# Kernel optimization log

Measured on AMD Instinct MI355X. Metric: run time of the kernel, lower is better.

Reference implementation:

```python
import jax, jax.numpy as jnp
import numpy as np
from math import sqrt

D = 512        # output_dim (layer_dims[-1])
H = 4          # num_heads
ATN = D // H   # atn_dim = 128
BERT_D = 768
B = 32         # number of graph pairs
NP = 4096
NH = 4096


def setup_inputs() -> dict:
    key = jax.random.key(0)
    ks = jax.random.split(key, 20)
    inp = {
        'ctx_p': jax.random.normal(ks[0], (NP, D), jnp.float32),
        'ctx_h': jax.random.normal(ks[1], (NH, D), jnp.float32),
        'lhs_p': jax.random.normal(ks[2], (NP, BERT_D), jnp.float32),
        'lhs_h': jax.random.normal(ks[3], (NH, BERT_D), jnp.float32),
        'batch_p': jnp.sort(jax.random.randint(ks[4], (NP,), 0, B)).astype(jnp.int64),
        'batch_h': jnp.sort(jax.random.randint(ks[5], (NH,), 0, B)).astype(jnp.int64),
        # learned parameters (stored [in, out])
        'Wq': jax.random.normal(ks[6], (D, D), jnp.float32) * 0.02,
        'bq': jnp.zeros((D,), jnp.float32),
        'Wk': jax.random.normal(ks[7], (D, D), jnp.float32) * 0.02,
        'bk': jnp.zeros((D,), jnp.float32),
        'Wv': jax.random.normal(ks[8], (BERT_D, BERT_D), jnp.float32) * 0.02,
        'bv': jnp.zeros((BERT_D,), jnp.float32),
        'W1': jax.random.normal(ks[9], (D + BERT_D, 256), jnp.float32) * 0.02,
        'b1': jnp.zeros((256,), jnp.float32),
        'W2': jax.random.normal(ks[10], (256, 128), jnp.float32) * 0.02,
        'ln_g': jnp.ones((128,), jnp.float32),
        'ln_b': jnp.zeros((128,), jnp.float32),
        'Wc': jax.random.normal(ks[11], (128, 3), jnp.float32) * 0.02,
        'bc': jnp.zeros((3,), jnp.float32),
    }
    return inp


def reference(ctx_p, ctx_h, lhs_p, lhs_h, batch_p, batch_h,
              Wq, bq, Wk, bk, Wv, bv, W1, b1, W2, ln_g, ln_b, Wc, bc):
    # q/k projections; torch code does .view(-1, atn_dim, num_heads) -> head is fastest axis
    qs = (ctx_h @ Wq + bq).reshape(-1, ATN, H)          # [nh, atn, H]
    ks = (ctx_p @ Wk + bk).reshape(-1, ATN, H)          # [np, atn, H]
    vs = (lhs_p @ Wv + bv).reshape(-1, H, BERT_D // H)  # [np, H, 768/H]

    atn = jnp.einsum('ndh,mdh->nmh', qs, ks) / sqrt(ATN)  # [nh, np, H]
    # faithful to original: positions where batch ids MATCH are set to -1e10
    mask_same = batch_h[:, None] == batch_p[None, :]       # [nh, np]
    atn = jnp.where(mask_same[:, :, None], jnp.float32(-1e10), atn)
    atn = jax.nn.softmax(atn, axis=1)                      # softmax over premise words m

    attended = jnp.einsum('nmh,mhd->nhd', atn, vs).reshape(-1, BERT_D)  # [nh, 768]

    feats = jnp.concatenate([ctx_h, lhs_h - attended], axis=1)  # [nh, D+768]
    h1 = jax.nn.gelu(feats @ W1 + b1, approximate=False)
    h2 = h1 @ W2                                                # Linear no bias
    mu = h2.mean(axis=-1, keepdims=True)
    var = ((h2 - mu) ** 2).mean(axis=-1, keepdims=True)
    h2 = (h2 - mu) * jax.lax.rsqrt(var + 1e-5) * ln_g + ln_b    # LayerNorm(128)

    # global_mean_pool over batch_h
    pooled = jax.ops.segment_sum(h2, batch_h, num_segments=B)
    counts = jax.ops.segment_sum(jnp.ones((h2.shape[0], 1), h2.dtype), batch_h, num_segments=B)
    pooled = pooled / jnp.maximum(counts, 1.0)

    return pooled @ Wc + bc  # [B, 3]
```

## Files before the change

kernel.cpp:

```cpp
#include <hip/hip_runtime.h>
#include <hip/hip_bf16.h>
#include <math.h>

#define NP_N 4096
#define NH_N 4096
#define D_N 512
#define BERT_N 768
#define H_N 4
#define B_N 32
#define SCL2 0.12754245006257576f

typedef __attribute__((ext_vector_type(8))) short short8;
typedef __attribute__((ext_vector_type(4))) float f32x4;
typedef __attribute__((ext_vector_type(4))) unsigned short ush4;
typedef __attribute__((ext_vector_type(4))) unsigned int uivec4;
typedef unsigned short ushort_t;

__device__ __forceinline__ void gl_lds16(const void* g, void* l) {
    __builtin_amdgcn_global_load_lds((const __attribute__((address_space(1))) void*)g,
                                     (__attribute__((address_space(3))) void*)l, 16, 0, 0);
}
__device__ __forceinline__ unsigned short f2bu(float f) {
    __hip_bfloat16 b = __float2bfloat16(f);
    return *reinterpret_cast<unsigned short*>(&b);
}
__device__ __forceinline__ float b2f(unsigned short u) {
    union { unsigned int i; float f; } x; x.i = ((unsigned int)u) << 16; return x.f;
}
__device__ __forceinline__ unsigned int pkbf(float a, float b) {
    union { __hip_bfloat162 h; unsigned int u; } x;
    x.h.x = __float2bfloat16(a);
    x.h.y = __float2bfloat16(b);
    return x.u;
}
__device__ __forceinline__ unsigned int sxor(unsigned int v, int m) {
    return (unsigned int)__shfl_xor((int)v, m);
}

__device__ __forceinline__ short8 mkfrag(uint2 u, uint2 v, bool hi, bool godd) {
    unsigned ux32 = sxor(u.x, 32), uy32 = sxor(u.y, 32);
    unsigned vx32 = sxor(v.x, 32), vy32 = sxor(v.y, 32);
    unsigned ax = hi ? vx32 : u.x, bx = hi ? v.x : ux32;
    unsigned ay = hi ? vy32 : u.y, by = hi ? v.y : uy32;
    unsigned sbx = sxor(bx, 16), sax = sxor(ax, 16);
    unsigned sby = sxor(by, 16), say = sxor(ay, 16);
    uivec4 w;
    w.x = godd ? sbx : ax;
    w.y = godd ? sby : ay;
    w.z = godd ? bx : sax;
    w.w = godd ? by : say;
    return __builtin_bit_cast(short8, w);
}

#define EW_BLOCKS 512
__global__ __launch_bounds__(256) void convert_all(
    const float* __restrict__ ctx_h, const float* __restrict__ ctx_p,
    const float* __restrict__ lhs_p,
    const float* __restrict__ Wq, const float* __restrict__ Wk,
    const float* __restrict__ Wv, const float* __restrict__ W1,
    const float* __restrict__ bq, const float* __restrict__ bk,
    ushort_t* __restrict__ ctxp_bf, ushort_t* __restrict__ lhsp_bf,
    ushort_t* __restrict__ feats,
    ushort_t* __restrict__ Wqt, ushort_t* __restrict__ Wkt,
    ushort_t* __restrict__ Wvt, ushort_t* __restrict__ W1t,
    float* __restrict__ bqp, float* __restrict__ bkp)
{
    const int bid = blockIdx.x, t = threadIdx.x;
    if (bid < EW_BLOCKS) {
        const long N0 = 524288, N1 = 1048576, TOT = 1835008;
        for (long i = (long)bid * 256 + t; i < TOT; i += (long)EW_BLOCKS * 256) {
            float4 v; ush4 o;
            if (i < N0) {
                long k = i;
                v = ((const float4*)ctx_h)[k];
                o[0] = f2bu(v.x); o[1] = f2bu(v.y); o[2] = f2bu(v.z); o[3] = f2bu(v.w);
                long n = k >> 7, c4 = k & 127;
                ((ush4*)feats)[n * 320 + c4] = o;
            } else if (i < N1) {
                long k = i - N0;
                v = ((const float4*)ctx_p)[k];
                o[0] = f2bu(v.x); o[1] = f2bu(v.y); o[2] = f2bu(v.z); o[3] = f2bu(v.w);
                ((ush4*)ctxp_bf)[k] = o;
            } else {
                long k = i - N1;
                v = ((const float4*)lhs_p)[k];
                o[0] = f2bu(v.x); o[1] = f2bu(v.y); o[2] = f2bu(v.z); o[3] = f2bu(v.w);
                ((ush4*)lhsp_bf)[k] = o;
            }
        }
        if (bid == 0) {
            for (int n = t; n < 512; n += 256) {
                int np = (n & 3) * 128 + (n >> 2);
                bqp[np] = bq[n] * SCL2;
                bkp[np] = bk[n];
            }
        }
        return;
    }
    int tb = bid - EW_BLOCKS;
    const float* src; ushort_t* dst; int K, N, tile, perm; float wscl;
    if (tb < 64)       { src = Wq; dst = Wqt; K = 512;  N = 512; tile = tb;       perm = 1; wscl = SCL2; }
    else if (tb < 128) { src = Wk; dst = Wkt; K = 512;  N = 512; tile = tb - 64;  perm = 1; wscl = 1.f; }
    else if (tb < 272) { src = Wv; dst = Wvt; K = 768;  N = 768; tile = tb - 128; perm = 0; wscl = 1.f; }
    else               { src = W1; dst = W1t; K = 1280; N = 256; tile = tb - 272; perm = 0; wscl = 1.f; }
    int ntn = N >> 6;
    int k0 = (tile / ntn) * 64, n0 = (tile % ntn) * 64;
    __shared__ float tl[64][65];
#pragma unroll
    for (int i = 0; i < 16; i++) {
        int idx = t + i * 256; int r = idx >> 6, c = idx & 63;
        tl[r][c] = src[(size_t)(k0 + r) * N + n0 + c];
    }
    __syncthreads();
#pragma unroll
    for (int i = 0; i < 16; i++) {
        int idx = t + i * 256; int r = idx >> 6, c = idx & 63;
        int n = n0 + r;
        int nr = perm ? ((n & 3) * 128 + (n >> 2)) : n;
        dst[(size_t)nr * K + k0 + c] = f2bu(tl[c][r] * wscl);
    }
}

template<int TM, int TN, int BIAS_ROW, int GELU>
__global__ __launch_bounds__(256) void gemm2(
    const ushort_t* __restrict__ A, int lda, const ushort_t* __restrict__ Bt,
    const float* __restrict__ bias, ushort_t* __restrict__ C,
    int M, int N, int K)
{
    constexpr int MF = TM / 32, NF = TN / 32;
    constexpr int AI = TM / 32, BI = TN / 32;
    __shared__ ushort_t As[2][TM * 64];
    __shared__ ushort_t Bs[2][TN * 64];
    const int t = threadIdx.x, w = t >> 6, lane = t & 63;
    const int lq = lane & 15, g = lane >> 4;
    const int wm = w >> 1, wn = w & 1;
    const int n0 = blockIdx.x * TN, m0 = blockIdx.y * TM;
    const int nsteps = K >> 6;

    f32x4 acc[MF][NF] = {};

    auto STAGE = [&](int buf, int k0) {
#pragma unroll
        for (int jj = 0; jj < AI; jj++) {
            int j = w * AI + jj;
            int r = j * 8 + (lane >> 3);
            int c = (lane & 7) * 16;
            int cs = c ^ ((r & 7) << 4);
            gl_lds16((const char*)A + ((size_t)(m0 + r) * lda + k0) * 2 + cs,
                     (void*)&As[buf][j * 512]);
        }
#pragma unroll
        for (int jj = 0; jj < BI; jj++) {
            int j = w * BI + jj;
            int r = j * 8 + (lane >> 3);
            int c = (lane & 7) * 16;
            int cs = c ^ ((r & 7) << 4);
            gl_lds16((const char*)Bt + ((size_t)(n0 + r) * K + k0) * 2 + cs,
                     (void*)&Bs[buf][j * 512]);
        }
    };

    STAGE(0, 0);
    asm volatile("s_waitcnt vmcnt(0)" ::: "memory");
    __builtin_amdgcn_s_barrier();
    int cur = 0;
    for (int s = 0; s < nsteps; s++) {
        if (s + 1 < nsteps) STAGE(cur ^ 1, (s + 1) * 64);
        const char* Ab = (const char*)&As[cur][0];
        const char* Bb = (const char*)&Bs[cur][0];
        const int swz = (lq & 7) << 4;
        short8 af[MF][2], bfr[NF][2];
#pragma unroll
        for (int mf = 0; mf < MF; mf++) {
            int r = wm * (TM / 2) + mf * 16 + lq;
#pragma unroll
            for (int ks = 0; ks < 2; ks++)
                af[mf][ks] = *(const short8*)(Ab + r * 128 + ((ks * 64 + g * 16) ^ swz));
        }
#pragma unroll
        for (int nf = 0; nf < NF; nf++) {
            int r = wn * (TN / 2) + nf * 16 + lq;
#pragma unroll
            for (int ks = 0; ks < 2; ks++)
                bfr[nf][ks] = *(const short8*)(Bb + r * 128 + ((ks * 64 + g * 16) ^ swz));
        }
        __builtin_amdgcn_s_setprio(1);
#pragma unroll
        for (int mf = 0; mf < MF; mf++)
#pragma unroll
            for (int nf = 0; nf < NF; nf++)
#pragma unroll
                for (int ks = 0; ks < 2; ks++)
                    acc[mf][nf] = __builtin_amdgcn_mfma_f32_16x16x32_bf16(
                        af[mf][ks], bfr[nf][ks], acc[mf][nf], 0, 0, 0);
        __builtin_amdgcn_s_setprio(0);
        asm volatile("s_waitcnt vmcnt(0)" ::: "memory");
        __builtin_amdgcn_s_barrier();
        cur ^= 1;
    }

#pragma unroll
    for (int mf = 0; mf < MF; mf++) {
#pragma unroll
        for (int nf = 0; nf < NF; nf++) {
            int ncol = n0 + wn * (TN / 2) + nf * 16 + lq;
            float bcol = BIAS_ROW ? 0.f : bias[ncol];
#pragma unroll
            for (int j = 0; j < 4; j++) {
                int mrow = m0 + wm * (TM / 2) + mf * 16 + 4 * g + j;
                float v = acc[mf][nf][j] + (BIAS_ROW ? bias[mrow] : bcol);
                if (GELU) v = 0.5f * v * (1.f + erff(v * 0.70710678118654752f));
                C[(size_t)mrow * N + ncol] = f2bu(v);
            }
        }
    }
}

__global__ __launch_bounds__(512, 2) void attn_mfma(
    const ushort_t* __restrict__ Qb,
    const ushort_t* __restrict__ Kb,
    const ushort_t* __restrict__ Vtb,
    const int* __restrict__ batch_h, const int* __restrict__ batch_p,
    ushort_t* __restrict__ Opart,
    float* __restrict__ ml)
{
    const int bid = blockIdx.x;
    const int h = (bid & 7) >> 1;
    const int s = bid & 1;
    const int n0 = (bid >> 3) * 128;

    __shared__ __align__(16) char smem[163840];

    const int t = threadIdx.x;
    const int w = t >> 6, o = w >> 2, wq = w & 3;
    const int lane = t & 63, lq = lane & 15, g = lane >> 4;
    const int lqm = (lq & 7) << 4;
    const bool hi = lane >= 32;
    const bool godd = (lane & 16) != 0;

    char* Kt0 = smem + (o * 2 + 0) * 16384;
    char* Kt1 = smem + (o * 2 + 1) * 16384;
    char* Vt0 = smem + 65536 + (o * 2 + 0) * 24576;
    char* Vt1 = smem + 65536 + (o * 2 + 1) * 24576;

    short8 qf[2][4];
    int bhq[2];
#pragma unroll
    for (int qg = 0; qg < 2; qg++) {
        const ushort_t* qrow = Qb + (size_t)(n0 + wq * 32 + qg * 16 + lq) * 512 + h * 128;
#pragma unroll
        for (int ks = 0; ks < 4; ks++)
            qf[qg][ks] = *(const short8*)(qrow + ks * 32 + g * 8);
        bhq[qg] = batch_h[n0 + wq * 32 + qg * 16 + lq];
    }

    f32x4 Ofr[2][12];
#pragma unroll
    for (int qg = 0; qg < 2; qg++)
#pragma unroll
        for (int nt = 0; nt < 12; nt++) Ofr[qg][nt] = (f32x4){0.f, 0.f, 0.f, 0.f};
    float m_run[2] = {-1e30f, -1e30f}, l_run[2] = {0.f, 0.f};

    const char* Kg = (const char*)Kb;
    const char* Vg = (const char*)Vtb;
    const int kb = s * 2048 + o * 1024;

    auto STAGE = [&](char* Kd, char* Vd, int m0k) {
#pragma unroll
        for (int jj = 0; jj < 4; jj++) {
            int j = wq * 4 + jj;
            int r = j * 4 + (lane >> 4);
            int c = (lane & 15) * 16;
            gl_lds16(Kg + (size_t)(m0k + r) * 1024 + h * 256 + (c ^ ((r & 7) << 4)),
                     Kd + j * 1024);
        }
#pragma unroll
        for (int jj = 0; jj < 6; jj++) {
            int j = wq * 6 + jj;
            int r = j * 8 + (lane >> 3);
            int c = (lane & 7) * 16;
            gl_lds16(Vg + ((size_t)(h * 192 + r) * 4096 + m0k) * 2 + (c ^ ((r & 7) << 4)),
                     Vd + j * 1024);
        }
    };

    STAGE(Kt0, Vt0, kb);
    asm volatile("s_waitcnt vmcnt(0)" ::: "memory");
    __builtin_amdgcn_s_barrier();
    int cur = 0;

    for (int tile = 0; tile < 16; tile++) {
        char* Kc = cur ? Kt1 : Kt0;
        char* Vc = cur ? Vt1 : Vt0;
        const int ktb = kb + tile * 64;

        int4 bp4[4];
#pragma unroll
        for (int mt = 0; mt < 4; mt++)
            bp4[mt] = *(const int4*)&batch_p[ktb + mt * 16 + 4 * g];

        if (tile + 1 < 16) STAGE(cur ? Kt0 : Kt1, cur ? Vt0 : Vt1, kb + (tile + 1) * 64);

        f32x4 S[2][4];
#pragma unroll
        for (int qg = 0; qg < 2; qg++)
#pragma unroll
            for (int mt = 0; mt < 4; mt++) S[qg][mt] = (f32x4){0.f, 0.f, 0.f, 0.f};
        __builtin_amdgcn_s_setprio(1);
#pragma unroll
        for (int mt = 0; mt < 4; mt++) {
            const char* rbase = Kc + (mt * 16 + lq) * 256;
#pragma unroll
            for (int ks = 0; ks < 4; ks++) {
                short8 kf = *(const short8*)(rbase + ((ks * 64 + g * 16) ^ lqm));
                S[0][mt] = __builtin_amdgcn_mfma_f32_16x16x32_bf16(kf, qf[0][ks], S[0][mt], 0, 0, 0);
                S[1][mt] = __builtin_amdgcn_mfma_f32_16x16x32_bf16(kf, qf[1][ks], S[1][mt], 0, 0, 0);
            }
        }
        __builtin_amdgcn_s_setprio(0);

        float pmax[2];
#pragma unroll
        for (int qg = 0; qg < 2; qg++) {
            float m = -1e30f;
#pragma unroll
            for (int mt = 0; mt < 4; mt++) {
                float v0 = (bp4[mt].x == bhq[qg]) ? -1e9f : S[qg][mt][0];
                float v1 = (bp4[mt].y == bhq[qg]) ? -1e9f : S[qg][mt][1];
                float v2 = (bp4[mt].z == bhq[qg]) ? -1e9f : S[qg][mt][2];
                float v3 = (bp4[mt].w == bhq[qg]) ? -1e9f : S[qg][mt][3];
                S[qg][mt][0] = v0; S[qg][mt][1] = v1; S[qg][mt][2] = v2; S[qg][mt][3] = v3;
                m = fmaxf(m, fmaxf(fmaxf(v0, v1), fmaxf(v2, v3)));
            }
            pmax[qg] = m;
        }
        bool ng = __all((pmax[0] <= m_run[0] + 8.f) && (pmax[1] <= m_run[1] + 8.f));
        if (!ng) {
#pragma unroll
            for (int qg = 0; qg < 2; qg++) {
                float mq = fmaxf(pmax[qg], m_run[qg]);
                mq = fmaxf(mq, __shfl_xor(mq, 16));
                mq = fmaxf(mq, __shfl_xor(mq, 32));
                float f = exp2f(m_run[qg] - mq);
                m_run[qg] = mq;
                l_run[qg] *= f;
                float fr0 = __shfl(f, 4 * g + 0);
                float fr1 = __shfl(f, 4 * g + 1);
                float fr2 = __shfl(f, 4 * g + 2);
                float fr3 = __shfl(f, 4 * g + 3);
#pragma unroll
                for (int nt = 0; nt < 12; nt++) {
                    Ofr[qg][nt][0] *= fr0; Ofr[qg][nt][1] *= fr1;
                    Ofr[qg][nt][2] *= fr2; Ofr[qg][nt][3] *= fr3;
                }
            }
        }

        uint2 P2[2][4];
#pragma unroll
        for (int qg = 0; qg < 2; qg++) {
            float lsum = 0.f;
#pragma unroll
            for (int mt = 0; mt < 4; mt++) {
                float e0 = exp2f(S[qg][mt][0] - m_run[qg]);
                float e1 = exp2f(S[qg][mt][1] - m_run[qg]);
                float e2 = exp2f(S[qg][mt][2] - m_run[qg]);
                float e3 = exp2f(S[qg][mt][3] - m_run[qg]);
                lsum += (e0 + e1) + (e2 + e3);
                P2[qg][mt].x = pkbf(e0, e1);
                P2[qg][mt].y = pkbf(e2, e3);
            }
            l_run[qg] += lsum;
        }

#pragma unroll
        for (int ks = 0; ks < 2; ks++) {
            short8 pf0 = mkfrag(P2[0][2 * ks], P2[0][2 * ks + 1], hi, godd);
            short8 pf1 = mkfrag(P2[1][2 * ks], P2[1][2 * ks + 1], hi, godd);
            __builtin_amdgcn_s_setprio(1);
#pragma unroll
            for (int nt = 0; nt < 12; nt++) {
                short8 vf = *(const short8*)(Vc + (nt * 16 + lq) * 128 + ((ks * 64 + g * 16) ^ lqm));
                Ofr[0][nt] = __builtin_amdgcn_mfma_f32_16x16x32_bf16(pf0, vf, Ofr[0][nt], 0, 0, 0);
                Ofr[1][nt] = __builtin_amdgcn_mfma_f32_16x16x32_bf16(pf1, vf, Ofr[1][nt], 0, 0, 0);
            }
            __builtin_amdgcn_s_setprio(0);
        }

        asm volatile("s_waitcnt vmcnt(0)" ::: "memory");
        __builtin_amdgcn_s_barrier();
        cur ^= 1;
    }

    float lt[2];
#pragma unroll
    for (int qg = 0; qg < 2; qg++) {
        float l = l_run[qg];
        l += __shfl_xor(l, 16);
        l += __shfl_xor(l, 32);
        lt[qg] = l;
    }

    const int tq = wq * 64 + lane;
    float* mOf = (float*)smem;
    float* mls = (float*)(smem + 98304);
    if (o == 1) {
#pragma unroll
        for (int qg = 0; qg < 2; qg++) {
#pragma unroll
            for (int nt = 0; nt < 12; nt++)
                *(f32x4*)(mOf + tq * 96 + qg * 48 + nt * 4) = Ofr[qg][nt];
            if (g == 0) {
                mls[(wq * 16 + lq) * 4 + qg * 2 + 0] = m_run[qg];
                mls[(wq * 16 + lq) * 4 + qg * 2 + 1] = lt[qg];
            }
        }
    }
    __syncthreads();
    if (o == 0) {
        const size_t plane = (size_t)(s * 4 + h) * 4096;
#pragma unroll
        for (int qg = 0; qg < 2; qg++) {
            float m1 = mls[(wq * 16 + lq) * 4 + qg * 2 + 0];
            float l1 = mls[(wq * 16 + lq) * 4 + qg * 2 + 1];
            float m = fmaxf(m_run[qg], m1);
            float a0 = exp2f(m_run[qg] - m), a1 = exp2f(m1 - m);
            float l = lt[qg] * a0 + l1 * a1;
            int qrow = n0 + wq * 32 + qg * 16;
            if (g == 0) {
                ml[(plane + qrow + lq) * 2 + 0] = m;
                ml[(plane + qrow + lq) * 2 + 1] = l;
            }
            float f0[4], f1[4];
#pragma unroll
            for (int j = 0; j < 4; j++) {
                f0[j] = __shfl(a0, 4 * g + j);
                f1[j] = __shfl(a1, 4 * g + j);
            }
#pragma unroll
            for (int nt = 0; nt < 12; nt++) {
                f32x4 o1 = *(f32x4*)(mOf + tq * 96 + qg * 48 + nt * 4);
#pragma unroll
                for (int j = 0; j < 4; j++) {
                    float val = Ofr[qg][nt][j] * f0[j] + o1[j] * f1[j];
                    Opart[(plane + qrow + 4 * g + j) * 192 + nt * 16 + lq] = f2bu(val);
                }
            }
        }
    }
}

__global__ __launch_bounds__(256) void combine_feats(
    const ushort_t* __restrict__ Opart, const float* __restrict__ ml,
    const float* __restrict__ lhs_h, ushort_t* __restrict__ feats)
{
    const int t = threadIdx.x;
#pragma unroll
    for (int i = 0; i < 4; i++) {
        int q = blockIdx.x * 4 + i;
#pragma unroll
        for (int it = 0; it < 3; it++) {
            int c = t + it * 256;
            int h = c / 192, vd = c - h * 192;
            size_t i0 = (size_t)h * 4096 + q;
            size_t i1 = (size_t)(4 + h) * 4096 + q;
            float m0 = ml[i0 * 2], l0 = ml[i0 * 2 + 1];
            float m1 = ml[i1 * 2], l1 = ml[i1 * 2 + 1];
            float m = fmaxf(m0, m1);
            float e0 = exp2f(m0 - m), e1 = exp2f(m1 - m);
            float linv = 1.f / (l0 * e0 + l1 * e1);
            float O = (b2f(Opart[i0 * 192 + vd]) * e0 + b2f(Opart[i1 * 192 + vd]) * e1) * linv;
            feats[(size_t)q * 1280 + 512 + c] = f2bu(lhs_h[(size_t)q * 768 + c] - O);
        }
    }
}

__global__ __launch_bounds__(256) void h2_ln(
    const ushort_t* __restrict__ h1, const float* __restrict__ W2,
    const float* __restrict__ ln_g, const float* __restrict__ ln_b,
    float* __restrict__ h2out)
{
    const int n0 = blockIdx.x * 8;
    const int t = threadIdx.x;
    __shared__ float h1s[8][256];
    __shared__ float h2s[8][128];

#pragma unroll
    for (int i = 0; i < 8; i++) {
        int idx = t + i * 256; int r = idx >> 8, c = idx & 255;
        h1s[r][c] = b2f(h1[(size_t)(n0 + r) * 256 + c]);
    }
    __syncthreads();

    {
        int o2 = t & 127, gq = t >> 7;
        float acc[4] = {};
        for (int k4 = 0; k4 < 64; k4++) {
            float w0 = W2[(size_t)(k4 * 4 + 0) * 128 + o2];
            float w1 = W2[(size_t)(k4 * 4 + 1) * 128 + o2];
            float w2 = W2[(size_t)(k4 * 4 + 2) * 128 + o2];
            float w3 = W2[(size_t)(k4 * 4 + 3) * 128 + o2];
#pragma unroll
            for (int q = 0; q < 4; q++) {
                float4 hh = *(const float4*)&h1s[gq * 4 + q][k4 * 4];
                acc[q] += hh.x * w0 + hh.y * w1 + hh.z * w2 + hh.w * w3;
            }
        }
#pragma unroll
        for (int q = 0; q < 4; q++) h2s[gq * 4 + q][o2] = acc[q];
    }
    __syncthreads();

    {
        int wv = t >> 6, lane = t & 63;
#pragma unroll
        for (int sx = 0; sx < 2; sx++) {
            int nd = wv * 2 + sx;
            float x0 = h2s[nd][lane], x1 = h2s[nd][lane + 64];
            float sum = x0 + x1;
#pragma unroll
            for (int off = 32; off; off >>= 1) sum += __shfl_xor(sum, off);
            float mu = sum * (1.f / 128.f);
            float d0 = x0 - mu, d1 = x1 - mu;
            float s2 = d0 * d0 + d1 * d1;
#pragma unroll
            for (int off = 32; off; off >>= 1) s2 += __shfl_xor(s2, off);
            float rstd = rsqrtf(s2 * (1.f / 128.f) + 1e-5f);
            size_t base = (size_t)(n0 + nd) * 128;
            h2out[base + lane]      = d0 * rstd * ln_g[lane] + ln_b[lane];
            h2out[base + lane + 64] = d1 * rstd * ln_g[lane + 64] + ln_b[lane + 64];
        }
    }
}

__global__ void ranges_kernel(const int* __restrict__ bh, int* __restrict__ lo,
                              int Nn, int Bn)
{
    int n = blockIdx.x * blockDim.x + threadIdx.x;
    if (n >= Nn) return;
    int b = bh[n];
    int prev = (n == 0) ? -1 : bh[n - 1];
    for (int bb = prev + 1; bb <= b; bb++) lo[bb] = n;
    if (n == Nn - 1) for (int bb = b + 1; bb <= Bn; bb++) lo[bb] = Nn;
}

__global__ __launch_bounds__(128) void pool_cls(
    const float* __restrict__ h2, const int* __restrict__ lo,
    const float* __restrict__ Wc, const float* __restrict__ bc,
    float* __restrict__ out)
{
    int b = blockIdx.x, t = threadIdx.x;
    int s = lo[b], e = lo[b + 1];
    float acc = 0.f;
    for (int n = s; n < e; n++) acc += h2[(size_t)n * 128 + t];
    float pooled = acc / fmaxf((float)(e - s), 1.f);
    __shared__ float red[128];
    for (int c = 0; c < 3; c++) {
        red[t] = pooled * Wc[t * 3 + c];
        __syncthreads();
        for (int off = 64; off > 0; off >>= 1) {
            if (t < off) red[t] += red[t + off];
            __syncthreads();
        }
        if (t == 0) out[b * 3 + c] = red[0] + bc[c];
        __syncthreads();
    }
}

extern "C" void kernel_launch(void* const* d_in, const int* in_sizes, int n_in,
                              void* d_out, int out_size, void* d_ws, size_t ws_size,
                              hipStream_t stream)
{
    const float* ctx_p  = (const float*)d_in[0];
    const float* ctx_h  = (const float*)d_in[1];
    const float* lhs_p  = (const float*)d_in[2];
    const float* lhs_h  = (const float*)d_in[3];
    const int*   batch_p = (const int*)d_in[4];
    const int*   batch_h = (const int*)d_in[5];
    const float* Wq = (const float*)d_in[6];
    const float* bq = (const float*)d_in[7];
    const float* Wk = (const float*)d_in[8];
    const float* bk = (const float*)d_in[9];
    const float* Wv = (const float*)d_in[10];
    const float* bv = (const float*)d_in[11];
    const float* W1 = (const float*)d_in[12];
    const float* b1 = (const float*)d_in[13];
    const float* W2 = (const float*)d_in[14];
    const float* ln_g = (const float*)d_in[15];
    const float* ln_b = (const float*)d_in[16];
    const float* Wc = (const float*)d_in[17];
    const float* bc = (const float*)d_in[18];
    float* out = (float*)d_out;

    ushort_t* u = (ushort_t*)d_ws;
    ushort_t* ctxp_bf = u;
    ushort_t* lhsp_bf = ctxp_bf + 2097152;
    ushort_t* Wqt  = lhsp_bf + 3145728;
    ushort_t* Wkt  = Wqt + 262144;
    ushort_t* Wvt  = Wkt + 262144;
    ushort_t* Opart = u;
    ushort_t* W1t  = Wvt + 589824;
    ushort_t* Qb   = W1t + 327680;
    ushort_t* Kb   = Qb + 2097152;
    ushort_t* Vtb  = Kb + 2097152;
    ushort_t* feats = Vtb + 3145728;
    ushort_t* h1   = feats + 5242880;
    float* ml  = (float*)(h1 + 1048576);
    float* h2  = ml + 65536;
    float* bqp = h2 + 524288;
    float* bkp = bqp + 512;
    int*   lo  = (int*)(bkp + 512);

    convert_all<<<864, 256, 0, stream>>>(
        ctx_h, ctx_p, lhs_p, Wq, Wk, Wv, W1, bq, bk,
        ctxp_bf, lhsp_bf, feats, Wqt, Wkt, Wvt, W1t, bqp, bkp);

    gemm2<128, 64, 0, 0><<<dim3(8, 32), 256, 0, stream>>>(feats, 1280, Wqt, bqp, Qb, NH_N, 512, 512);
    gemm2<128, 64, 0, 0><<<dim3(8, 32), 256, 0, stream>>>(ctxp_bf, 512, Wkt, bkp, Kb, NP_N, 512, 512);
    gemm2<128, 64, 1, 0><<<dim3(64, 6), 256, 0, stream>>>(Wvt, 768, lhsp_bf, bv, Vtb, 768, NP_N, 768);

    attn_mfma<<<256, 512, 0, stream>>>(Qb, Kb, Vtb, batch_h, batch_p, Opart, ml);

    combine_feats<<<1024, 256, 0, stream>>>(Opart, ml, lhs_h, feats);

    gemm2<64, 64, 0, 1><<<dim3(4, 64), 256, 0, stream>>>(feats, 1280, W1t, b1, h1, NH_N, 256, 1280);

    h2_ln<<<512, 256, 0, stream>>>(h1, W2, ln_g, ln_b, h2);
    ranges_kernel<<<16, 256, 0, stream>>>(batch_h, lo, NH_N, B_N);
    pool_cls<<<B_N, 128, 0, stream>>>(h2, lo, Wc, bc, out);
}
```

Measured before the change: 202.8 us.

## Merge Q/K/V projection GEMMs into one launch and drop ranges kernel

Replaces the three separate projection GEMM launches with one 64x64-tiled kernel that picks its operands by block index, and splits the elementwise conversion into fixed per-tensor block ranges. The separate ranges kernel is removed; pool_cls now binary-searches segment bounds in batch_h itself. The GEMMs switch to smaller tiles and plain __syncthreads, dropping the explicit vmcnt waits and setprio hints. The aim is fewer launches and better occupancy, at the cost of less data reuse per tile and possibly weaker latency hiding.

```diff
diff --git a/kernel.cpp b/kernel.cpp
--- a/kernel.cpp
+++ b/kernel.cpp
@@ -52,7 +52,6 @@
     return __builtin_bit_cast(short8, w);
 }
 
-#define EW_BLOCKS 512
 __global__ __launch_bounds__(256) void convert_all(
     const float* __restrict__ ctx_h, const float* __restrict__ ctx_p,
     const float* __restrict__ lhs_p,
@@ -66,27 +65,12 @@
     float* __restrict__ bqp, float* __restrict__ bkp)
 {
     const int bid = blockIdx.x, t = threadIdx.x;
-    if (bid < EW_BLOCKS) {
-        const long N0 = 524288, N1 = 1048576, TOT = 1835008;
-        for (long i = (long)bid * 256 + t; i < TOT; i += (long)EW_BLOCKS * 256) {
-            float4 v; ush4 o;
-            if (i < N0) {
-                long k = i;
-                v = ((const float4*)ctx_h)[k];
-                o[0] = f2bu(v.x); o[1] = f2bu(v.y); o[2] = f2bu(v.z); o[3] = f2bu(v.w);
-                long n = k >> 7, c4 = k & 127;
-                ((ush4*)feats)[n * 320 + c4] = o;
-            } else if (i < N1) {
-                long k = i - N0;
-                v = ((const float4*)ctx_p)[k];
-                o[0] = f2bu(v.x); o[1] = f2bu(v.y); o[2] = f2bu(v.z); o[3] = f2bu(v.w);
-                ((ush4*)ctxp_bf)[k] = o;
-            } else {
-                long k = i - N1;
-                v = ((const float4*)lhs_p)[k];
-                o[0] = f2bu(v.x); o[1] = f2bu(v.y); o[2] = f2bu(v.z); o[3] = f2bu(v.w);
-                ((ush4*)lhsp_bf)[k] = o;
-            }
+    if (bid < 128) {
+        for (long k = (long)bid * 256 + t; k < 524288; k += 128 * 256) {
+            float4 v = ((const float4*)ctx_h)[k];
+            ush4 o; o[0] = f2bu(v.x); o[1] = f2bu(v.y); o[2] = f2bu(v.z); o[3] = f2bu(v.w);
+            long n = k >> 7, c4 = k & 127;
+            ((ush4*)feats)[n * 320 + c4] = o;
         }
         if (bid == 0) {
             for (int n = t; n < 512; n += 256) {
@@ -97,7 +81,23 @@
         }
         return;
     }
-    int tb = bid - EW_BLOCKS;
+    if (bid < 256) {
+        for (long k = (long)(bid - 128) * 256 + t; k < 524288; k += 128 * 256) {
+            float4 v = ((const float4*)ctx_p)[k];
+            ush4 o; o[0] = f2bu(v.x); o[1] = f2bu(v.y); o[2] = f2bu(v.z); o[3] = f2bu(v.w);
+            ((ush4*)ctxp_bf)[k] = o;
+        }
+        return;
+    }
+    if (bid < 448) {
+        for (long k = (long)(bid - 256) * 256 + t; k < 786432; k += 192 * 256) {
+            float4 v = ((const float4*)lhs_p)[k];
+            ush4 o; o[0] = f2bu(v.x); o[1] = f2bu(v.y); o[2] = f2bu(v.z); o[3] = f2bu(v.w);
+            ((ush4*)lhsp_bf)[k] = o;
+        }
+        return;
+    }
+    int tb = bid - 448;
     const float* src; ushort_t* dst; int K, N, tile, perm; float wscl;
     if (tb < 64)       { src = Wq; dst = Wqt; K = 512;  N = 512; tile = tb;       perm = 1; wscl = SCL2; }
     else if (tb < 128) { src = Wk; dst = Wkt; K = 512;  N = 512; tile = tb - 64;  perm = 1; wscl = 1.f; }
@@ -121,95 +121,183 @@
     }
 }
 
-template<int TM, int TN, int BIAS_ROW, int GELU>
-__global__ __launch_bounds__(256) void gemm2(
-    const ushort_t* __restrict__ A, int lda, const ushort_t* __restrict__ Bt,
-    const float* __restrict__ bias, ushort_t* __restrict__ C,
-    int M, int N, int K)
+__global__ __launch_bounds__(256) void gemm_qkv(
+    const ushort_t* __restrict__ feats, const ushort_t* __restrict__ ctxp,
+    const ushort_t* __restrict__ Wqt, const ushort_t* __restrict__ Wkt,
+    const ushort_t* __restrict__ Wvt, const ushort_t* __restrict__ lhsp,
+    const float* __restrict__ bqp, const float* __restrict__ bkp,
+    const float* __restrict__ bv,
+    ushort_t* __restrict__ Qb, ushort_t* __restrict__ Kb,
+    ushort_t* __restrict__ Vtb)
 {
-    constexpr int MF = TM / 32, NF = TN / 32;
-    constexpr int AI = TM / 32, BI = TN / 32;
-    __shared__ ushort_t As[2][TM * 64];
-    __shared__ ushort_t Bs[2][TN * 64];
+    int b = blockIdx.x;
+    const ushort_t *A, *Bt; const float* bias; ushort_t* C;
+    int lda, N, K, m0, n0, bias_row;
+    if (b < 512) {
+        A = feats; lda = 1280; Bt = Wqt; bias = bqp; C = Qb;
+        N = 512; K = 512; bias_row = 0;
+        n0 = (b & 7) * 64; m0 = (b >> 3) * 64;
+    } else if (b < 1024) {
+        b -= 512;
+        A = ctxp; lda = 512; Bt = Wkt; bias = bkp; C = Kb;
+        N = 512; K = 512; bias_row = 0;
+        n0 = (b & 7) * 64; m0 = (b >> 3) * 64;
+    } else {
+        b -= 1024;
+        A = Wvt; lda = 768; Bt = lhsp; bias = bv; C = Vtb;
+        N = 4096; K = 768; bias_row = 1;
+        n0 = (b & 63) * 64; m0 = (b >> 6) * 64;
+    }
+    const int nsteps = K >> 6;
+
+    __shared__ ushort_t As[2][64 * 64];
+    __shared__ ushort_t Bs[2][64 * 64];
     const int t = threadIdx.x, w = t >> 6, lane = t & 63;
     const int lq = lane & 15, g = lane >> 4;
     const int wm = w >> 1, wn = w & 1;
-    const int n0 = blockIdx.x * TN, m0 = blockIdx.y * TM;
-    const int nsteps = K >> 6;
-
-    f32x4 acc[MF][NF] = {};
+
+    f32x4 acc[2][2] = {};
 
     auto STAGE = [&](int buf, int k0) {
 #pragma unroll
-        for (int jj = 0; jj < AI; jj++) {
-            int j = w * AI + jj;
+        for (int jj = 0; jj < 2; jj++) {
+            int j = w * 2 + jj;
             int r = j * 8 + (lane >> 3);
             int c = (lane & 7) * 16;
             int cs = c ^ ((r & 7) << 4);
             gl_lds16((const char*)A + ((size_t)(m0 + r) * lda + k0) * 2 + cs,
                      (void*)&As[buf][j * 512]);
-        }
-#pragma unroll
-        for (int jj = 0; jj < BI; jj++) {
-            int j = w * BI + jj;
-            int r = j * 8 + (lane >> 3);
-            int c = (lane & 7) * 16;
-            int cs = c ^ ((r & 7) << 4);
             gl_lds16((const char*)Bt + ((size_t)(n0 + r) * K + k0) * 2 + cs,
                      (void*)&Bs[buf][j * 512]);
         }
     };
 
     STAGE(0, 0);
-    asm volatile("s_waitcnt vmcnt(0)" ::: "memory");
-    __builtin_amdgcn_s_barrier();
+    __syncthreads();
     int cur = 0;
     for (int s = 0; s < nsteps; s++) {
         if (s + 1 < nsteps) STAGE(cur ^ 1, (s + 1) * 64);
         const char* Ab = (const char*)&As[cur][0];
         const char* Bb = (const char*)&Bs[cur][0];
         const int swz = (lq & 7) << 4;
-        short8 af[MF][2], bfr[NF][2];
-#pragma unroll
-        for (int mf = 0; mf < MF; mf++) {
-            int r = wm * (TM / 2) + mf * 16 + lq;
+        short8 af[2][2], bfr[2][2];
+#pragma unroll
+        for (int mf = 0; mf < 2; mf++) {
+            int r = wm * 32 + mf * 16 + lq;
 #pragma unroll
             for (int ks = 0; ks < 2; ks++)
                 af[mf][ks] = *(const short8*)(Ab + r * 128 + ((ks * 64 + g * 16) ^ swz));
         }
 #pragma unroll
-        for (int nf = 0; nf < NF; nf++) {
-            int r = wn * (TN / 2) + nf * 16 + lq;
+        for (int nf = 0; nf < 2; nf++) {
+            int r = wn * 32 + nf * 16 + lq;
 #pragma unroll
             for (int ks = 0; ks < 2; ks++)
                 bfr[nf][ks] = *(const short8*)(Bb + r * 128 + ((ks * 64 + g * 16) ^ swz));
         }
-        __builtin_amdgcn_s_setprio(1);
-#pragma unroll
-        for (int mf = 0; mf < MF; mf++)
-#pragma unroll
-            for (int nf = 0; nf < NF; nf++)
+#pragma unroll
+        for (int mf = 0; mf < 2; mf++)
+#pragma unroll
+            for (int nf = 0; nf < 2; nf++)
 #pragma unroll
                 for (int ks = 0; ks < 2; ks++)
                     acc[mf][nf] = __builtin_amdgcn_mfma_f32_16x16x32_bf16(
                         af[mf][ks], bfr[nf][ks], acc[mf][nf], 0, 0, 0);
-        __builtin_amdgcn_s_setprio(0);
-        asm volatile("s_waitcnt vmcnt(0)" ::: "memory");
-        __builtin_amdgcn_s_barrier();
+        __syncthreads();
         cur ^= 1;
     }
 
 #pragma unroll
-    for (int mf = 0; mf < MF; mf++) {
-#pragma unroll
-        for (int nf = 0; nf < NF; nf++) {
-            int ncol = n0 + wn * (TN / 2) + nf * 16 + lq;
-            float bcol = BIAS_ROW ? 0.f : bias[ncol];
+    for (int mf = 0; mf < 2; mf++) {
+#pragma unroll
+        for (int nf = 0; nf < 2; nf++) {
+            int ncol = n0 + wn * 32 + nf * 16 + lq;
+            float bcol = bias_row ? 0.f : bias[ncol];
 #pragma unroll
             for (int j = 0; j < 4; j++) {
-                int mrow = m0 + wm * (TM / 2) + mf * 16 + 4 * g + j;
-                float v = acc[mf][nf][j] + (BIAS_ROW ? bias[mrow] : bcol);
-                if (GELU) v = 0.5f * v * (1.f + erff(v * 0.70710678118654752f));
+                int mrow = m0 + wm * 32 + mf * 16 + 4 * g + j;
+                float v = acc[mf][nf][j] + (bias_row ? bias[mrow] : bcol);
+                C[(size_t)mrow * N + ncol] = f2bu(v);
+            }
+        }
+    }
+}
+
+__global__ __launch_bounds__(256) void gemm_mlp1(
+    const ushort_t* __restrict__ A, int lda, const ushort_t* __restrict__ Bt,
+    const float* __restrict__ bias, ushort_t* __restrict__ C,
+    int M, int N, int K)
+{
+    __shared__ ushort_t As[2][64 * 64];
+    __shared__ ushort_t Bs[2][64 * 64];
+    const int t = threadIdx.x, w = t >> 6, lane = t & 63;
+    const int lq = lane & 15, g = lane >> 4;
+    const int wm = w >> 1, wn = w & 1;
+    const int n0 = blockIdx.x * 64, m0 = blockIdx.y * 64;
+    const int nsteps = K >> 6;
+
+    f32x4 acc[2][2] = {};
+
+    auto STAGE = [&](int buf, int k0) {
+#pragma unroll
+        for (int jj = 0; jj < 2; jj++) {
+            int j = w * 2 + jj;
+            int r = j * 8 + (lane >> 3);
+            int c = (lane & 7) * 16;
+            int cs = c ^ ((r & 7) << 4);
+            gl_lds16((const char*)A + ((size_t)(m0 + r) * lda + k0) * 2 + cs,
+                     (void*)&As[buf][j * 512]);
+            gl_lds16((const char*)Bt + ((size_t)(n0 + r) * K + k0) * 2 + cs,
+                     (void*)&Bs[buf][j * 512]);
+        }
+    };
+
+    STAGE(0, 0);
+    __syncthreads();
+    int cur = 0;
+    for (int s = 0; s < nsteps; s++) {
+        if (s + 1 < nsteps) STAGE(cur ^ 1, (s + 1) * 64);
+        const char* Ab = (const char*)&As[cur][0];
+        const char* Bb = (const char*)&Bs[cur][0];
+        const int swz = (lq & 7) << 4;
+        short8 af[2][2], bfr[2][2];
+#pragma unroll
+        for (int mf = 0; mf < 2; mf++) {
+            int r = wm * 32 + mf * 16 + lq;
+#pragma unroll
+            for (int ks = 0; ks < 2; ks++)
+                af[mf][ks] = *(const short8*)(Ab + r * 128 + ((ks * 64 + g * 16) ^ swz));
+        }
+#pragma unroll
+        for (int nf = 0; nf < 2; nf++) {
+            int r = wn * 32 + nf * 16 + lq;
+#pragma unroll
+            for (int ks = 0; ks < 2; ks++)
+                bfr[nf][ks] = *(const short8*)(Bb + r * 128 + ((ks * 64 + g * 16) ^ swz));
+        }
+#pragma unroll
+        for (int mf = 0; mf < 2; mf++)
+#pragma unroll
+            for (int nf = 0; nf < 2; nf++)
+#pragma unroll
+                for (int ks = 0; ks < 2; ks++)
+                    acc[mf][nf] = __builtin_amdgcn_mfma_f32_16x16x32_bf16(
+                        af[mf][ks], bfr[nf][ks], acc[mf][nf], 0, 0, 0);
+        __syncthreads();
+        cur ^= 1;
+    }
+
+#pragma unroll
+    for (int mf = 0; mf < 2; mf++) {
+#pragma unroll
+        for (int nf = 0; nf < 2; nf++) {
+            int ncol = n0 + wn * 32 + nf * 16 + lq;
+            float bcol = bias[ncol];
+#pragma unroll
+            for (int j = 0; j < 4; j++) {
+                int mrow = m0 + wm * 32 + mf * 16 + 4 * g + j;
+                float v = acc[mf][nf][j] + bcol;
+                v = 0.5f * v * (1.f + erff(v * 0.70710678118654752f));
                 C[(size_t)mrow * N + ncol] = f2bu(v);
             }
         }
@@ -533,24 +621,24 @@
     }
 }
 
-__global__ void ranges_kernel(const int* __restrict__ bh, int* __restrict__ lo,
-                              int Nn, int Bn)
-{
-    int n = blockIdx.x * blockDim.x + threadIdx.x;
-    if (n >= Nn) return;
-    int b = bh[n];
-    int prev = (n == 0) ? -1 : bh[n - 1];
-    for (int bb = prev + 1; bb <= b; bb++) lo[bb] = n;
-    if (n == Nn - 1) for (int bb = b + 1; bb <= Bn; bb++) lo[bb] = Nn;
-}
-
 __global__ __launch_bounds__(128) void pool_cls(
-    const float* __restrict__ h2, const int* __restrict__ lo,
+    const float* __restrict__ h2, const int* __restrict__ batch_h,
     const float* __restrict__ Wc, const float* __restrict__ bc,
     float* __restrict__ out)
 {
     int b = blockIdx.x, t = threadIdx.x;
-    int s = lo[b], e = lo[b + 1];
+    __shared__ int bounds[2];
+    if (t < 2) {
+        int target = b + t;
+        int lo = 0, hi = NH_N;
+        while (lo < hi) {
+            int mid = (lo + hi) >> 1;
+            if (batch_h[mid] < target) lo = mid + 1; else hi = mid;
+        }
+        bounds[t] = lo;
+    }
+    __syncthreads();
+    int s = bounds[0], e = bounds[1];
     float acc = 0.f;
     for (int n = s; n < e; n++) acc += h2[(size_t)n * 128 + t];
     float pooled = acc / fmaxf((float)(e - s), 1.f);
@@ -609,23 +697,20 @@
     float* h2  = ml + 65536;
     float* bqp = h2 + 524288;
     float* bkp = bqp + 512;
-    int*   lo  = (int*)(bkp + 512);
-
-    convert_all<<<864, 256, 0, stream>>>(
+
+    convert_all<<<800, 256, 0, stream>>>(
         ctx_h, ctx_p, lhs_p, Wq, Wk, Wv, W1, bq, bk,
         ctxp_bf, lhsp_bf, feats, Wqt, Wkt, Wvt, W1t, bqp, bkp);
 
-    gemm2<128, 64, 0, 0><<<dim3(8, 32), 256, 0, stream>>>(feats, 1280, Wqt, bqp, Qb, NH_N, 512, 512);
-    gemm2<128, 64, 0, 0><<<dim3(8, 32), 256, 0, stream>>>(ctxp_bf, 512, Wkt, bkp, Kb, NP_N, 512, 512);
-    gemm2<128, 64, 1, 0><<<dim3(64, 6), 256, 0, stream>>>(Wvt, 768, lhsp_bf, bv, Vtb, 768, NP_N, 768);
+    gemm_qkv<<<1792, 256, 0, stream>>>(
+        feats, ctxp_bf, Wqt, Wkt, Wvt, lhsp_bf, bqp, bkp, bv, Qb, Kb, Vtb);
 
     attn_mfma<<<256, 512, 0, stream>>>(Qb, Kb, Vtb, batch_h, batch_p, Opart, ml);
 
     combine_feats<<<1024, 256, 0, stream>>>(Opart, ml, lhs_h, feats);
 
-    gemm2<64, 64, 0, 1><<<dim3(4, 64), 256, 0, stream>>>(feats, 1280, W1t, b1, h1, NH_N, 256, 1280);
+    gemm_mlp1<<<dim3(4, 64), 256, 0, stream>>>(feats, 1280, W1t, b1, h1, NH_N, 256, 1280);
 
     h2_ln<<<512, 256, 0, stream>>>(h1, W2, ln_g, ln_b, h2);
-    ranges_kernel<<<16, 256, 0, stream>>>(batch_h, lo, NH_N, B_N);
-    pool_cls<<<B_N, 128, 0, stream>>>(h2, lo, Wc, bc, out);
-}
+    pool_cls<<<B_N, 128, 0, stream>>>(h2, batch_h, Wc, bc, out);
+}
```

Measured after the change: 193.2 us. 1.05x faster.
